# Optimization experiments

Measured on AMD Instinct MI355X. Metric: run time of the kernel, lower is better.

The kernel has to match this reference:

```python
import jax, jax.numpy as jnp
import numpy as np

DIM = 1024
STATE = 16
K = 4
INNER = 2048
BATCH = 4
SEQ = 2048
EPS = 1e-6


def silu(x):
    return x * jax.nn.sigmoid(x)


def setup_inputs() -> dict:
    key = jax.random.key(0)
    ks = jax.random.split(key, 8)
    g = lambda k, s, sc: jax.random.normal(k, s, dtype=jnp.float32) * sc
    return {
        "x": jax.random.normal(ks[0], (BATCH, SEQ, DIM), dtype=jnp.float32),
        "w_norm": jnp.ones((DIM,), jnp.float32),
        "W_in": g(ks[1], (2 * INNER, DIM), 0.02),
        "conv_w": g(ks[2], (INNER, K), 0.2),  # depthwise conv kernel
        "conv_b": jnp.zeros((INNER,), jnp.float32),
        "W_dt": g(ks[3], (INNER, INNER), 0.02),
        "b_dt": jnp.zeros((INNER,), jnp.float32),
        "W_B": g(ks[4], (STATE, INNER), 0.02),
        "W_C": g(ks[5], (STATE, INNER), 0.02),
        "A_log": jnp.log(jnp.broadcast_to(jnp.arange(1, STATE + 1, dtype=jnp.float32), (INNER, STATE))),
        "D": jnp.ones((INNER,), jnp.float32),
        "W_out": g(ks[6], (DIM, INNER), 0.02),
    }


def reference(x, w_norm, W_in, conv_w, conv_b, W_dt, b_dt, W_B, W_C, A_log, D, W_out):
    b, L, d = x.shape
    # RMSNorm
    x_norm = x * jax.lax.rsqrt(jnp.mean(x * x, axis=-1, keepdims=True) + EPS) * w_norm
    # input projection and split
    x_and_res = x_norm @ W_in.T  # (b, L, 2*inner)
    x_inner, res = jnp.split(x_and_res, 2, axis=-1)
    # causal depthwise conv1d (pad left K-1, kernel per channel)
    xp = jnp.pad(x_inner, ((0, 0), (K - 1, 0), (0, 0)))
    x_conv = sum(xp[:, j:j + L, :] * conv_w[:, j] for j in range(K)) + conv_b
    x_conv = silu(x_conv)
    # SSM parameters
    dt = jax.nn.softplus(x_conv @ W_dt.T + b_dt)  # (b, L, inner)
    Bm = x_conv @ W_B.T  # (b, L, state)
    Cm = x_conv @ W_C.T  # (b, L, state)
    A = -jnp.exp(A_log)  # (inner, state)

    def step(h, inp):
        dt_t, B_t, C_t, xc_t = inp  # (b,inner),(b,state),(b,state),(b,inner)
        dA = jnp.exp(A * dt_t[..., None])  # (b, inner, state)
        h = dA * h + (dt_t[..., None] * B_t[:, None, :]) * xc_t[..., None]
        y_t = jnp.einsum('bis,bs->bi', h, C_t) + D * xc_t
        return h, y_t

    h0 = jnp.zeros((b, INNER, STATE), x.dtype)
    xs = (dt.transpose(1, 0, 2), Bm.transpose(1, 0, 2), Cm.transpose(1, 0, 2), x_conv.transpose(1, 0, 2))
    _, y = jax.lax.scan(step, h0, xs)  # y: (L, b, inner)
    y = y.transpose(1, 0, 2)
    y = y * silu(res)
    return y @ W_out.T
```

## Files before the change

### kernel.cpp

```cpp
#include <hip/hip_runtime.h>


typedef __bf16 bf16;
typedef __attribute__((ext_vector_type(8))) __bf16 bf16x8;
typedef __attribute__((ext_vector_type(4))) float f32x4;

#define DIM   1024
#define STATE 16
#define INNER 2048
#define BATCH 4
#define SEQ   2048
#define ROWS  (BATCH * SEQ)
#define N1    (2 * INNER)
#define NBC   2176
#define CHUNK 128
#define NC    (SEQ / CHUNK)
#define PF2   4

#define GLOAD_LDS16(g, l)                                                  \
  __builtin_amdgcn_global_load_lds(                                        \
      (const __attribute__((address_space(1))) unsigned int*)(g),          \
      (__attribute__((address_space(3))) unsigned int*)(l), 16, 0, 0)

__global__ void ws_report_kernel(float* out, float wssz, float need) {
  if (threadIdx.x == 0) { out[0] = wssz; out[1] = need; }
}

__global__ __launch_bounds__(256) void rmsnorm_kernel(
    const float* __restrict__ x, const float* __restrict__ w,
    bf16* __restrict__ out) {
  const int row = blockIdx.x;
  const int t = threadIdx.x;
  const float4 v = ((const float4*)(x + (long)row * DIM))[t];
  float ss = v.x * v.x + v.y * v.y + v.z * v.z + v.w * v.w;
#pragma unroll
  for (int off = 32; off > 0; off >>= 1) ss += __shfl_xor(ss, off, 64);
  __shared__ float red[4];
  if ((t & 63) == 0) red[t >> 6] = ss;
  __syncthreads();
  const float tot = red[0] + red[1] + red[2] + red[3];
  const float scale = rsqrtf(tot * (1.0f / DIM) + 1e-6f);
  const float4 wv = ((const float4*)w)[t];
  bf16* o = out + (long)row * DIM + t * 4;
  o[0] = (bf16)(v.x * scale * wv.x);
  o[1] = (bf16)(v.y * scale * wv.y);
  o[2] = (bf16)(v.z * scale * wv.z);
  o[3] = (bf16)(v.w * scale * wv.w);
}

__global__ __launch_bounds__(256) void cvt_bf16_kernel(
    const float* __restrict__ src, bf16* __restrict__ dst, int n) {
  const int i = blockIdx.x * 256 + threadIdx.x;
  if (i < n) dst[i] = (bf16)src[i];
}

__global__ __launch_bounds__(256) void build_wdtbc_kernel(
    const float* __restrict__ Wdt, const float* __restrict__ WB,
    const float* __restrict__ WC, bf16* __restrict__ dst) {
  const long i = (long)blockIdx.x * 256 + threadIdx.x;
  const long r = i >> 11;
  const long k = i & (INNER - 1);
  float v = 0.0f;
  if (r < 2048) v = Wdt[r * INNER + k];
  else if (r < 2064) v = WB[(r - 2048) * INNER + k];
  else if (r < 2080) v = WC[(r - 2064) * INNER + k];
  dst[i] = (bf16)v;
}

__global__ __launch_bounds__(256) void build_a2_kernel(
    const float* __restrict__ A_log, float* __restrict__ A2) {
  const int i = blockIdx.x * 256 + threadIdx.x;
  A2[i] = -__expf(A_log[i]) * 1.4426950408889634f;
}

template <int EPI>
__global__ __launch_bounds__(256) void gemm_bf16_kernel(
    const bf16* __restrict__ A, const bf16* __restrict__ B,
    float* __restrict__ Cf, float* __restrict__ Cf2,
    bf16* __restrict__ Cb, bf16* __restrict__ Cb2,
    const float* __restrict__ bias, int nx, int N, int K) {
  __shared__ __align__(16) bf16 As[128 * 32];
  __shared__ __align__(16) bf16 Bs[128 * 32];
  const int tid = threadIdx.x;
  const int lane = tid & 63;
  const int wave = tid >> 6;

  const int per = gridDim.x >> 3;
  const int lin = (blockIdx.x & 7) * per + (blockIdx.x >> 3);
  const int row_t = lin / nx;
  const int col_t = lin - row_t * nx;
  const long row0 = (long)row_t * 128;
  const long col0 = (long)col_t * 128;

  const int wr = (wave >> 1) * 64;
  const int wc = (wave & 1) * 64;

  f32x4 acc[4][4];
#pragma unroll
  for (int i = 0; i < 4; i++)
#pragma unroll
    for (int j = 0; j < 4; j++) acc[i][j] = (f32x4){0.f, 0.f, 0.f, 0.f};

  const int srow = tid >> 2;
  const int scol = (tid & 3) * 8;
  const bf16* gA0 = A + (row0 + srow) * (long)K + scol;
  const bf16* gA1 = A + (row0 + srow + 64) * (long)K + scol;
  const bf16* gB0 = B + (col0 + srow) * (long)K + scol;
  const bf16* gB1 = B + (col0 + srow + 64) * (long)K + scol;
  bf16* lA0 = As + wave * 512 + lane * 8;
  bf16* lA1 = As + 64 * 32 + wave * 512 + lane * 8;
  bf16* lB0 = Bs + wave * 512 + lane * 8;
  bf16* lB1 = Bs + 64 * 32 + wave * 512 + lane * 8;

  const int fm = lane & 15;
  const int fk = (lane >> 4) * 8;

  for (int k0 = 0; k0 < K; k0 += 32) {
    GLOAD_LDS16(gA0 + k0, lA0);
    GLOAD_LDS16(gA1 + k0, lA1);
    GLOAD_LDS16(gB0 + k0, lB0);
    GLOAD_LDS16(gB1 + k0, lB1);
    __syncthreads();
    bf16x8 af[4], bfv[4];
#pragma unroll
    for (int i = 0; i < 4; i++)
      af[i] = *(const bf16x8*)(As + (wr + i * 16 + fm) * 32 + fk);
#pragma unroll
    for (int j = 0; j < 4; j++)
      bfv[j] = *(const bf16x8*)(Bs + (wc + j * 16 + fm) * 32 + fk);
#pragma unroll
    for (int i = 0; i < 4; i++)
#pragma unroll
      for (int j = 0; j < 4; j++)
        acc[i][j] = __builtin_amdgcn_mfma_f32_16x16x32_bf16(
            af[i], bfv[j], acc[i][j], 0, 0, 0);
    __syncthreads();
  }

  const int er = (lane >> 4) * 4;
  const int ec = lane & 15;
#pragma unroll
  for (int i = 0; i < 4; i++) {
#pragma unroll
    for (int j = 0; j < 4; j++) {
      const long col = col0 + wc + j * 16 + ec;
      const long rw = row0 + wr + i * 16 + er;
#pragma unroll
      for (int r = 0; r < 4; r++) {
        const float v = acc[i][j][r];
        const long row = rw + r;
        if (EPI == 0) {
          Cf[row * (long)N + col] = v;
        } else if (EPI == 1) {
          if (col0 < 2048) {
            float z = v + bias[col];
            z = (z > 20.0f) ? z : log1pf(__expf(z));
            Cf[row * 2048 + col] = z;
          } else if (col < 2080) {
            Cf2[row * 32 + (col - 2048)] = v;
          }
        } else {
          if (col0 < 2048) {
            Cb[row * 2048 + col] = (bf16)v;
          } else {
            const float s = v / (1.0f + __expf(-v));
            Cb2[row * 2048 + (col - 2048)] = (bf16)s;
          }
        }
      }
    }
  }
}

__global__ __launch_bounds__(256) void conv_silu_kernel(
    const bf16* __restrict__ xin, const float* __restrict__ conv_w,
    const float* __restrict__ conv_b, bf16* __restrict__ xc16) {
  const int c = blockIdx.x * 256 + threadIdx.x;
  const int r = blockIdx.y;
  const int l = r & (SEQ - 1);
  const float4 w = *(const float4*)(conv_w + c * 4);
  float acc = conv_b[c];
#pragma unroll
  for (int j = 0; j < 4; j++) {
    const int lp = l - 3 + j;
    const float xv = (lp >= 0) ? (float)xin[(long)(r - 3 + j) * INNER + c] : 0.0f;
    acc += xv * ((const float*)&w)[j];
  }
  const float s = acc / (1.0f + __expf(-acc));
  xc16[(long)r * INNER + c] = (bf16)s;
}

__global__ __launch_bounds__(256) void scan_pass1_kernel(
    const float* __restrict__ dtm, const float* __restrict__ bc,
    const bf16* __restrict__ xc, const float* __restrict__ A2,
    float* __restrict__ hend, float* __restrict__ dtsum) {
  const int ch = blockIdx.x * 256 + threadIdx.x;
  const int c = blockIdx.y;
  const int b = blockIdx.z;
  const long row0 = (long)b * SEQ + (long)c * CHUNK;

  float a2[16];
#pragma unroll
  for (int q = 0; q < 4; q++) {
    const float4 t = ((const float4*)(A2 + (long)ch * 16))[q];
    a2[q * 4 + 0] = t.x; a2[q * 4 + 1] = t.y;
    a2[q * 4 + 2] = t.z; a2[q * 4 + 3] = t.w;
  }
  float h[16];
#pragma unroll
  for (int s = 0; s < 16; s++) h[s] = 0.0f;
  float dts = 0.0f;

  float dtq[PF2], xcq[PF2];
#pragma unroll
  for (int p = 0; p < PF2; p++) {
    const long r2 = row0 + p;
    dtq[p] = dtm[r2 * INNER + ch];
    xcq[p] = (float)xc[r2 * INNER + ch];
  }
  for (int l0 = 0; l0 <= CHUNK - 2 * PF2; l0 += PF2) {
#pragma unroll
    for (int p = 0; p < PF2; p++) {
      const float dt = dtq[p], xcv = xcq[p];
      const long rp = row0 + l0 + p + PF2;
      dtq[p] = dtm[rp * INNER + ch];
      xcq[p] = (float)xc[rp * INNER + ch];
      const long r = row0 + l0 + p;
      float Bv[16];
#pragma unroll
      for (int k = 0; k < 16; k++) Bv[k] = bc[r * 32 + k];
      dts += dt;
      const float u = dt * xcv;
#pragma unroll
      for (int s = 0; s < 16; s++)
        h[s] = exp2f(a2[s] * dt) * h[s] + Bv[s] * u;
    }
  }
#pragma unroll
  for (int p = 0; p < PF2; p++) {
    const float dt = dtq[p], xcv = xcq[p];
    const long r = row0 + CHUNK - PF2 + p;
    float Bv[16];
#pragma unroll
    for (int k = 0; k < 16; k++) Bv[k] = bc[r * 32 + k];
    dts += dt;
    const float u = dt * xcv;
#pragma unroll
    for (int s = 0; s < 16; s++)
      h[s] = exp2f(a2[s] * dt) * h[s] + Bv[s] * u;
  }

  const long cb = (long)(b * NC + c);
#pragma unroll
  for (int s = 0; s < 16; s++) hend[(cb * 16 + s) * INNER + ch] = h[s];
  dtsum[cb * INNER + ch] = dts;
}

__global__ __launch_bounds__(256) void scan_combine_kernel(
    float* __restrict__ hio, const float* __restrict__ dtsum,
    const float* __restrict__ A2) {
  const int idx = blockIdx.x * 256 + threadIdx.x;
  const int ch = idx & (INNER - 1);
  const int s = (idx >> 11) & 15;
  const int b = idx >> 15;
  const float a2 = A2[(long)ch * 16 + s];
  float H = 0.0f;
  for (int c = 0; c < NC; c++) {
    const long cb = (long)(b * NC + c);
    const long o = (cb * 16 + s) * INNER + ch;
    const float he = hio[o];
    const float ds = dtsum[cb * INNER + ch];
    hio[o] = H;
    H = exp2f(a2 * ds) * H + he;
  }
}

__global__ __launch_bounds__(256) void scan_pass3_kernel(
    const float* __restrict__ dtm, const float* __restrict__ bc,
    const bf16* __restrict__ xc, const bf16* __restrict__ rs,
    const float* __restrict__ A2, const float* __restrict__ Dv,
    const float* __restrict__ hstart, bf16* __restrict__ y) {
  const int ch = blockIdx.x * 256 + threadIdx.x;
  const int c = blockIdx.y;
  const int b = blockIdx.z;
  const long row0 = (long)b * SEQ + (long)c * CHUNK;

  float a2[16];
#pragma unroll
  for (int q = 0; q < 4; q++) {
    const float4 t = ((const float4*)(A2 + (long)ch * 16))[q];
    a2[q * 4 + 0] = t.x; a2[q * 4 + 1] = t.y;
    a2[q * 4 + 2] = t.z; a2[q * 4 + 3] = t.w;
  }
  const float d = Dv[ch];
  const long cb = (long)(b * NC + c);
  float h[16];
#pragma unroll
  for (int s = 0; s < 16; s++) h[s] = hstart[(cb * 16 + s) * INNER + ch];

  float dtq[PF2], xcq[PF2], rsq[PF2];
#pragma unroll
  for (int p = 0; p < PF2; p++) {
    const long r2 = row0 + p;
    dtq[p] = dtm[r2 * INNER + ch];
    xcq[p] = (float)xc[r2 * INNER + ch];
    rsq[p] = (float)rs[r2 * INNER + ch];
  }
  for (int l0 = 0; l0 <= CHUNK - 2 * PF2; l0 += PF2) {
#pragma unroll
    for (int p = 0; p < PF2; p++) {
      const float dt = dtq[p], xcv = xcq[p], rsv = rsq[p];
      const long rp = row0 + l0 + p + PF2;
      dtq[p] = dtm[rp * INNER + ch];
      xcq[p] = (float)xc[rp * INNER + ch];
      rsq[p] = (float)rs[rp * INNER + ch];
      const long r = row0 + l0 + p;
      float Bv[16], Cv[16];
#pragma unroll
      for (int k = 0; k < 16; k++) Bv[k] = bc[r * 32 + k];
#pragma unroll
      for (int k = 0; k < 16; k++) Cv[k] = bc[r * 32 + 16 + k];
      const float u = dt * xcv;
      float yv = d * xcv;
#pragma unroll
      for (int s = 0; s < 16; s++) {
        h[s] = exp2f(a2[s] * dt) * h[s] + Bv[s] * u;
        yv += h[s] * Cv[s];
      }
      y[r * INNER + ch] = (bf16)(yv * rsv);
    }
  }
#pragma unroll
  for (int p = 0; p < PF2; p++) {
    const float dt = dtq[p], xcv = xcq[p], rsv = rsq[p];
    const long r = row0 + CHUNK - PF2 + p;
    float Bv[16], Cv[16];
#pragma unroll
    for (int k = 0; k < 16; k++) Bv[k] = bc[r * 32 + k];
#pragma unroll
    for (int k = 0; k < 16; k++) Cv[k] = bc[r * 32 + 16 + k];
    const float u = dt * xcv;
    float yv = d * xcv;
#pragma unroll
    for (int s = 0; s < 16; s++) {
      h[s] = exp2f(a2[s] * dt) * h[s] + Bv[s] * u;
      yv += h[s] * Cv[s];
    }
    y[r * INNER + ch] = (bf16)(yv * rsv);
  }
}

extern "C" void kernel_launch(void* const* d_in, const int* in_sizes, int n_in,
                              void* d_out, int out_size, void* d_ws,
                              size_t ws_size, hipStream_t stream) {
  (void)in_sizes; (void)n_in; (void)out_size;
  const float* x      = (const float*)d_in[0];
  const float* w_norm = (const float*)d_in[1];
  const float* W_in   = (const float*)d_in[2];
  const float* conv_w = (const float*)d_in[3];
  const float* conv_b = (const float*)d_in[4];
  const float* W_dt   = (const float*)d_in[5];
  const float* b_dt   = (const float*)d_in[6];
  const float* W_B    = (const float*)d_in[7];
  const float* W_C    = (const float*)d_in[8];
  const float* A_log  = (const float*)d_in[9];
  const float* Dv     = (const float*)d_in[10];
  const float* W_out  = (const float*)d_in[11];
  float* out = (float*)d_out;

  const size_t MB = 1024ull * 1024ull;
  char* base = (char*)d_ws;
  bf16*  xnorm  = (bf16*)(base + 0);
  bf16*  win_b  = (bf16*)(base + 16 * MB);
  bf16*  xin_b  = (bf16*)(base + 24 * MB);
  float* dtm    = (float*)(base + 0);
  float* bcm    = (float*)(base + 64 * MB);
  bf16*  res_b  = (bf16*)(base + 65 * MB);
  bf16*  xc_b   = (bf16*)(base + 97 * MB);
  bf16*  wdtbcb = (bf16*)(base + 129 * MB);
  float* hend   = (float*)(base + 129 * MB);
  float* dtsum  = (float*)(base + 137 * MB);
  char*  p2     = base + 129 * MB + (size_t)NBC * INNER * 2;
  bf16*  wout_b = (bf16*)p2;
  float* A2     = (float*)(p2 + (size_t)DIM * INNER * 2);
  bf16*  yb     = (bf16*)(p2 + (size_t)DIM * INNER * 2 +
                          (size_t)INNER * STATE * 4);
  const size_t NEEDED = (size_t)((char*)yb - base) + (size_t)ROWS * INNER * 2;

  if (ws_size < NEEDED) {
    ws_report_kernel<<<1, 64, 0, stream>>>(out, (float)ws_size, (float)NEEDED);
    return;
  }

  rmsnorm_kernel<<<ROWS, 256, 0, stream>>>(x, w_norm, xnorm);

  cvt_bf16_kernel<<<(N1 * DIM) / 256, 256, 0, stream>>>(W_in, win_b, N1 * DIM);
  build_wdtbc_kernel<<<(NBC * INNER) / 256, 256, 0, stream>>>(W_dt, W_B, W_C,
                                                              wdtbcb);
  cvt_bf16_kernel<<<(DIM * INNER) / 256, 256, 0, stream>>>(W_out, wout_b,
                                                           DIM * INNER);
  build_a2_kernel<<<(INNER * STATE) / 256, 256, 0, stream>>>(A_log, A2);

  gemm_bf16_kernel<2><<<(N1 / 128) * (ROWS / 128), 256, 0, stream>>>(
      xnorm, win_b, nullptr, nullptr, xin_b, res_b, nullptr, N1 / 128, N1,
      DIM);

  conv_silu_kernel<<<dim3(INNER / 256, ROWS), 256, 0, stream>>>(
      xin_b, conv_w, conv_b, xc_b);

  gemm_bf16_kernel<1><<<(NBC / 128) * (ROWS / 128), 256, 0, stream>>>(
      xc_b, wdtbcb, dtm, bcm, nullptr, nullptr, b_dt, NBC / 128, NBC, INNER);

  scan_pass1_kernel<<<dim3(INNER / 256, NC, BATCH), 256, 0, stream>>>(
      dtm, bcm, xc_b, A2, hend, dtsum);
  scan_combine_kernel<<<(BATCH * 16 * INNER) / 256, 256, 0, stream>>>(
      hend, dtsum, A2);
  scan_pass3_kernel<<<dim3(INNER / 256, NC, BATCH), 256, 0, stream>>>(
      dtm, bcm, xc_b, res_b, A2, Dv, hend, yb);

  gemm_bf16_kernel<0><<<(DIM / 128) * (ROWS / 128), 256, 0, stream>>>(
      yb, wout_b, out, nullptr, nullptr, nullptr, nullptr, DIM / 128, DIM,
      INNER);
}
```

Measured before the change: 713.6 us.

## Use 256x256 tiled bf16 GEMM with LDS double buffering for in-proj and dt/B/C GEMMs

Adds a new GEMM kernel with 256x256 output tiles, 512 threads (8 waves), and double-buffered LDS filled by direct global-to-LDS loads. The MFMA work is split into phases with staggered prefetch, barriers and s_setprio. It replaces the 128x128 GEMM for the input projection and the dt/B/C projection, keeping the fused epilogues (SiLU on res, softplus+bias, B/C output). The aim is more operand reuse per tile and loads overlapped with compute. The costs are 128KB of LDS per block, which limits occupancy, and the row clamp needed to handle B's padded 2176-row matrix.

```diff
diff --git a/kernel.cpp b/kernel.cpp
--- a/kernel.cpp
+++ b/kernel.cpp
@@ -71,6 +71,198 @@
     const float* __restrict__ A_log, float* __restrict__ A2) {
   const int i = blockIdx.x * 256 + threadIdx.x;
   A2[i] = -__expf(A_log[i]) * 1.4426950408889634f;
+}
+
+#define MFMA_PHASE(I0, N0)                                                    \
+  __builtin_amdgcn_s_barrier();                                               \
+  asm volatile("s_waitcnt lgkmcnt(0)" ::: "memory");                          \
+  __builtin_amdgcn_s_setprio(1);                                              \
+  _Pragma("unroll") for (int i_ = 0; i_ < 4; ++i_)                            \
+  _Pragma("unroll") for (int n_ = 0; n_ < 2; ++n_)                            \
+  _Pragma("unroll") for (int k_ = 0; k_ < 2; ++k_)                            \
+      acc[(I0) + i_][(N0) + n_] = __builtin_amdgcn_mfma_f32_16x16x32_bf16(    \
+          afr[i_][k_], bfr[(N0) + n_][k_], acc[(I0) + i_][(N0) + n_], 0, 0,   \
+          0);                                                                 \
+  __builtin_amdgcn_s_setprio(0);                                              \
+  __builtin_amdgcn_s_barrier();
+
+template <int EPI, int K, int NX>
+__global__ __launch_bounds__(512, 2) void gemm256_kernel(
+    const bf16* __restrict__ A, const bf16* __restrict__ B,
+    float* __restrict__ Cf, float* __restrict__ Cf2,
+    bf16* __restrict__ Cb, bf16* __restrict__ Cb2,
+    const float* __restrict__ bias, int Bmax) {
+  __shared__ __align__(16) char lds[2][65536];
+  const int tid = threadIdx.x;
+  const int lane = tid & 63;
+  const int wave = tid >> 6;
+  const int wm = wave >> 2;
+  const int wn = wave & 3;
+
+  const int per = gridDim.x >> 3;
+  const int lin = (blockIdx.x & 7) * per + (blockIdx.x >> 3);
+  const int row_t = lin / NX;
+  const int col_t = lin - row_t * NX;
+  const long row0 = (long)row_t * 256;
+  const long col0 = (long)col_t * 256;
+
+  const int srow = tid >> 3;
+  const int scb = (tid & 7) * 16;
+  const int sswz = scb ^ ((srow & 7) << 4);
+  const char* gA = (const char*)A + (row0 + srow) * (long)(2 * K) + sswz;
+  const char* gB = (const char*)B + sswz;
+  long brow[4];
+#pragma unroll
+  for (int q = 0; q < 4; ++q) {
+    long r = col0 + q * 64 + srow;
+    brow[q] = (r > (long)Bmax ? (long)Bmax : r) * (long)(2 * K);
+  }
+
+#define STG_A(bb, q, kbyte)                                                   \
+  GLOAD_LDS16(gA + (long)(q) * 64 * (2 * K) + (kbyte),                        \
+              lds[bb] + (q) * 8192 + srow * 128 + scb)
+#define STG_B(bb, q, kbyte)                                                   \
+  GLOAD_LDS16(gB + brow[q] + (kbyte),                                         \
+              lds[bb] + 32768 + (q) * 8192 + srow * 128 + scb)
+
+  const int fm = lane & 15;
+  const int fq = lane >> 4;
+  const int swz = (fm & 7) << 4;
+  const int ck0 = (fq * 16) ^ swz;
+  const int ck1 = (fq * 16 + 64) ^ swz;
+  const int aro = (wm * 128 + fm) * 128;
+  const int bro = (wn * 64 + fm) * 128;
+
+  f32x4 acc[8][4];
+#pragma unroll
+  for (int i = 0; i < 8; ++i)
+#pragma unroll
+    for (int n = 0; n < 4; ++n) acc[i][n] = (f32x4){0.f, 0.f, 0.f, 0.f};
+  bf16x8 afr[4][2], bfr[4][2];
+
+  const int NT = K / 64;
+#pragma unroll
+  for (int q = 0; q < 4; ++q) STG_A(0, q, 0);
+#pragma unroll
+  for (int q = 0; q < 4; ++q) STG_B(0, q, 0);
+
+  for (int t = 0; t < NT; ++t) {
+    const int c = t & 1;
+    const int nb = c ^ 1;
+    const char* Ac = lds[c];
+    const char* Bc = lds[c] + 32768;
+    const long kb = (long)(t + 1) * 128;
+    const bool nx = (t + 1 < NT);
+    if (nx) {
+      STG_A(nb, 0, kb);
+      STG_A(nb, 1, kb);
+      asm volatile("s_waitcnt vmcnt(2)" ::: "memory");
+    } else {
+      asm volatile("s_waitcnt vmcnt(0)" ::: "memory");
+    }
+    __builtin_amdgcn_s_barrier();
+    asm volatile("" ::: "memory");
+#pragma unroll
+    for (int i = 0; i < 4; ++i) {
+      afr[i][0] = *(const bf16x8*)(Ac + aro + i * 2048 + ck0);
+      afr[i][1] = *(const bf16x8*)(Ac + aro + i * 2048 + ck1);
+    }
+#pragma unroll
+    for (int n = 0; n < 2; ++n) {
+      bfr[n][0] = *(const bf16x8*)(Bc + bro + n * 2048 + ck0);
+      bfr[n][1] = *(const bf16x8*)(Bc + bro + n * 2048 + ck1);
+    }
+    if (nx) { STG_A(nb, 2, kb); STG_A(nb, 3, kb); }
+    MFMA_PHASE(0, 0)
+#pragma unroll
+    for (int n = 2; n < 4; ++n) {
+      bfr[n][0] = *(const bf16x8*)(Bc + bro + n * 2048 + ck0);
+      bfr[n][1] = *(const bf16x8*)(Bc + bro + n * 2048 + ck1);
+    }
+    if (nx) { STG_B(nb, 0, kb); STG_B(nb, 1, kb); }
+    MFMA_PHASE(0, 2)
+#pragma unroll
+    for (int i = 0; i < 4; ++i) {
+      afr[i][0] = *(const bf16x8*)(Ac + aro + 8192 + i * 2048 + ck0);
+      afr[i][1] = *(const bf16x8*)(Ac + aro + 8192 + i * 2048 + ck1);
+    }
+    if (nx) { STG_B(nb, 2, kb); STG_B(nb, 3, kb); }
+    MFMA_PHASE(4, 2)
+    __builtin_amdgcn_s_setprio(1);
+#pragma unroll
+    for (int i = 0; i < 4; ++i)
+#pragma unroll
+      for (int n = 0; n < 2; ++n)
+#pragma unroll
+        for (int kk = 0; kk < 2; ++kk)
+          acc[4 + i][n] = __builtin_amdgcn_mfma_f32_16x16x32_bf16(
+              afr[i][kk], bfr[n][kk], acc[4 + i][n], 0, 0, 0);
+    __builtin_amdgcn_s_setprio(0);
+    __builtin_amdgcn_s_barrier();
+    asm volatile("" ::: "memory");
+  }
+#undef STG_A
+#undef STG_B
+
+  const int er = fq * 4;
+  const long rbase = row0 + wm * 128;
+  const long cbase = col0 + wn * 64;
+  if (EPI == 2) {
+    if (col0 < 2048) {
+#pragma unroll
+      for (int i = 0; i < 8; ++i)
+#pragma unroll
+        for (int n = 0; n < 4; ++n) {
+          const long col = cbase + n * 16 + fm;
+          const long rw = rbase + i * 16 + er;
+#pragma unroll
+          for (int r = 0; r < 4; ++r)
+            Cb[(rw + r) * 2048 + col] = (bf16)acc[i][n][r];
+        }
+    } else {
+#pragma unroll
+      for (int i = 0; i < 8; ++i)
+#pragma unroll
+        for (int n = 0; n < 4; ++n) {
+          const long col = cbase + n * 16 + fm - 2048;
+          const long rw = rbase + i * 16 + er;
+#pragma unroll
+          for (int r = 0; r < 4; ++r) {
+            const float v = acc[i][n][r];
+            const float s = v / (1.0f + __expf(-v));
+            Cb2[(rw + r) * 2048 + col] = (bf16)s;
+          }
+        }
+    }
+  } else {
+    if (col0 < 2048) {
+#pragma unroll
+      for (int i = 0; i < 8; ++i)
+#pragma unroll
+        for (int n = 0; n < 4; ++n) {
+          const long col = cbase + n * 16 + fm;
+          const float bs = bias[col];
+          const long rw = rbase + i * 16 + er;
+#pragma unroll
+          for (int r = 0; r < 4; ++r) {
+            float z = acc[i][n][r] + bs;
+            z = (z > 20.0f) ? z : log1pf(__expf(z));
+            Cf[(rw + r) * 2048 + col] = z;
+          }
+        }
+    } else if (wn == 0) {
+#pragma unroll
+      for (int i = 0; i < 8; ++i)
+#pragma unroll
+        for (int n = 0; n < 2; ++n) {
+          const long col = n * 16 + fm;
+          const long rw = rbase + i * 16 + er;
+#pragma unroll
+          for (int r = 0; r < 4; ++r)
+            Cf2[(rw + r) * 32 + col] = acc[i][n][r];
+        }
+    }
+  }
 }
 
 template <int EPI>
@@ -401,15 +593,14 @@
                                                            DIM * INNER);
   build_a2_kernel<<<(INNER * STATE) / 256, 256, 0, stream>>>(A_log, A2);
 
-  gemm_bf16_kernel<2><<<(N1 / 128) * (ROWS / 128), 256, 0, stream>>>(
-      xnorm, win_b, nullptr, nullptr, xin_b, res_b, nullptr, N1 / 128, N1,
-      DIM);
+  gemm256_kernel<2, 1024, 16><<<512, 512, 0, stream>>>(
+      xnorm, win_b, nullptr, nullptr, xin_b, res_b, nullptr, N1 - 1);
 
   conv_silu_kernel<<<dim3(INNER / 256, ROWS), 256, 0, stream>>>(
       xin_b, conv_w, conv_b, xc_b);
 
-  gemm_bf16_kernel<1><<<(NBC / 128) * (ROWS / 128), 256, 0, stream>>>(
-      xc_b, wdtbcb, dtm, bcm, nullptr, nullptr, b_dt, NBC / 128, NBC, INNER);
+  gemm256_kernel<1, 2048, 9><<<288, 512, 0, stream>>>(
+      xc_b, wdtbcb, dtm, bcm, nullptr, nullptr, b_dt, NBC - 1);
 
   scan_pass1_kernel<<<dim3(INNER / 256, NC, BATCH), 256, 0, stream>>>(
       dtm, bcm, xc_b, A2, hend, dtsum);
```

Measured after the change: 648.9 us. 1.1x faster.

## Add 256x256 multi-buffered GEMM kernel and split dt/BC projection

Applied to the files above, without the earlier changes.

Introduces a 512-thread GEMM with 256x256 tiles, a 4-stage LDS ring filled by direct global-to-LDS loads, XOR swizzling, and priority hints around MFMA bursts. It is used for the input projection, the dt projection and the output projection. The dt GEMM is split from the B/C projection, so the padded 2176-wide tile no longer wastes work. The small B/C GEMM now runs as a separate narrow launch. The goal is more operand reuse per tile and better latency hiding than the 128x128 single-buffered kernel, at the cost of more registers and fewer blocks (128 for the output GEMM).

```diff
diff --git a/kernel.cpp b/kernel.cpp
--- a/kernel.cpp
+++ b/kernel.cpp
@@ -54,16 +54,15 @@
   if (i < n) dst[i] = (bf16)src[i];
 }
 
-__global__ __launch_bounds__(256) void build_wdtbc_kernel(
-    const float* __restrict__ Wdt, const float* __restrict__ WB,
-    const float* __restrict__ WC, bf16* __restrict__ dst) {
-  const long i = (long)blockIdx.x * 256 + threadIdx.x;
-  const long r = i >> 11;
-  const long k = i & (INNER - 1);
+__global__ __launch_bounds__(256) void build_wbc_kernel(
+    const float* __restrict__ WB, const float* __restrict__ WC,
+    bf16* __restrict__ dst) {
+  const int i = blockIdx.x * 256 + threadIdx.x;
+  const int r = i >> 11;
+  const int k = i & (INNER - 1);
   float v = 0.0f;
-  if (r < 2048) v = Wdt[r * INNER + k];
-  else if (r < 2064) v = WB[(r - 2048) * INNER + k];
-  else if (r < 2080) v = WC[(r - 2064) * INNER + k];
+  if (r < 16) v = WB[r * INNER + k];
+  else if (r < 32) v = WC[(r - 16) * INNER + k];
   dst[i] = (bf16)v;
 }
 
@@ -73,12 +72,173 @@
   A2[i] = -__expf(A_log[i]) * 1.4426950408889634f;
 }
 
+template <int EPI, int K, int NX>
+__global__ __launch_bounds__(512, 2) void gemm256_kernel(
+    const bf16* __restrict__ A, const bf16* __restrict__ B,
+    float* __restrict__ Cf, bf16* __restrict__ Cb, bf16* __restrict__ Cb2,
+    const float* __restrict__ bias) {
+  __shared__ __align__(16) char lds[4][32768];
+  const int tid = threadIdx.x;
+  const int lane = tid & 63;
+  const int wave = tid >> 6;
+  const int wm = wave >> 2;
+  const int wn = wave & 3;
+
+  const int per = gridDim.x >> 3;
+  const int lin = (blockIdx.x & 7) * per + (blockIdx.x >> 3);
+  const int row_t = lin / NX;
+  const int col_t = lin - row_t * NX;
+  const long row0 = (long)row_t * 256;
+  const long col0 = (long)col_t * 256;
+
+  const int srow = tid >> 2;
+  const int scb = (tid & 3) * 16;
+  const int ssw = scb ^ (((srow >> 1) & 3) << 4);
+  const char* gA = (const char*)A + (row0 + srow) * (long)(2 * K) + ssw;
+  const char* gB = (const char*)B + (col0 + srow) * (long)(2 * K) + ssw;
+
+#define STG_A(bb, r, tt)                                                      \
+  GLOAD_LDS16(gA + (long)(r) * 128 * (2 * K) + (long)(tt) * 64,               \
+              lds[bb] + (r) * 8192 + srow * 64 + scb)
+#define STG_B(bb, r, tt)                                                      \
+  GLOAD_LDS16(gB + (long)(r) * 128 * (2 * K) + (long)(tt) * 64,               \
+              lds[bb] + 16384 + (r) * 8192 + srow * 64 + scb)
+
+  const int fm = lane & 15;
+  const int fq = lane >> 4;
+  const int ck = (fq * 16) ^ (((fm >> 1) & 3) << 4);
+  const int aro = (wm * 128 + fm) * 64;
+  const int bro = (wn * 64 + fm) * 64;
+
+  f32x4 acc[8][4];
+#pragma unroll
+  for (int i = 0; i < 8; ++i)
+#pragma unroll
+    for (int n = 0; n < 4; ++n) acc[i][n] = (f32x4){0.f, 0.f, 0.f, 0.f};
+  bf16x8 afr[4], bfr[4];
+
+  const int NT = K / 32;
+#pragma unroll
+  for (int t = 0; t < 3; ++t) {
+    STG_A(t, 0, t); STG_A(t, 1, t);
+    STG_B(t, 0, t); STG_B(t, 1, t);
+  }
+  asm volatile("s_waitcnt vmcnt(8)" ::: "memory");
+  __builtin_amdgcn_s_barrier();
+
+  for (int t = 0; t < NT; ++t) {
+    const int c = t & 3;
+    const int pb = (t + 3) & 3;
+    const char* Ac = lds[c];
+    const char* Bc = lds[c] + 16384;
+    const bool pf = (t + 3) < NT;
+#pragma unroll
+    for (int i = 0; i < 4; ++i)
+      afr[i] = *(const bf16x8*)(Ac + aro + i * 1024 + ck);
+#pragma unroll
+    for (int n = 0; n < 4; ++n)
+      bfr[n] = *(const bf16x8*)(Bc + bro + n * 1024 + ck);
+    if (pf) { STG_A(pb, 0, t + 3); STG_A(pb, 1, t + 3); }
+    __builtin_amdgcn_s_barrier();
+    asm volatile("s_waitcnt lgkmcnt(0)" ::: "memory");
+    __builtin_amdgcn_s_setprio(1);
+#pragma unroll
+    for (int i = 0; i < 4; ++i)
+#pragma unroll
+      for (int n = 0; n < 4; ++n)
+        acc[i][n] = __builtin_amdgcn_mfma_f32_16x16x32_bf16(
+            afr[i], bfr[n], acc[i][n], 0, 0, 0);
+    __builtin_amdgcn_s_setprio(0);
+    __builtin_amdgcn_s_barrier();
+#pragma unroll
+    for (int i = 0; i < 4; ++i)
+      afr[i] = *(const bf16x8*)(Ac + aro + (i + 4) * 1024 + ck);
+    if (pf) { STG_B(pb, 0, t + 3); STG_B(pb, 1, t + 3); }
+    __builtin_amdgcn_s_barrier();
+    asm volatile("s_waitcnt lgkmcnt(0)" ::: "memory");
+    __builtin_amdgcn_s_setprio(1);
+#pragma unroll
+    for (int i = 0; i < 4; ++i)
+#pragma unroll
+      for (int n = 0; n < 4; ++n)
+        acc[4 + i][n] = __builtin_amdgcn_mfma_f32_16x16x32_bf16(
+            afr[i], bfr[n], acc[4 + i][n], 0, 0, 0);
+    __builtin_amdgcn_s_setprio(0);
+    if (t < NT - 3) {
+      asm volatile("s_waitcnt vmcnt(8)" ::: "memory");
+    } else if (t == NT - 3) {
+      asm volatile("s_waitcnt vmcnt(4)" ::: "memory");
+    } else if (t == NT - 2) {
+      asm volatile("s_waitcnt vmcnt(0)" ::: "memory");
+    }
+    __builtin_amdgcn_s_barrier();
+  }
+#undef STG_A
+#undef STG_B
+
+  const int er = fq * 4;
+  const long rbase = row0 + wm * 128;
+  const long cbase = col0 + wn * 64;
+  if (EPI == 0) {
+    const long Nn = 256 * NX;
+#pragma unroll
+    for (int i = 0; i < 8; ++i)
+#pragma unroll
+      for (int n = 0; n < 4; ++n) {
+        const long col = cbase + n * 16 + fm;
+        const long rw = rbase + i * 16 + er;
+#pragma unroll
+        for (int r = 0; r < 4; ++r) Cf[(rw + r) * Nn + col] = acc[i][n][r];
+      }
+  } else if (EPI == 1) {
+#pragma unroll
+    for (int i = 0; i < 8; ++i)
+#pragma unroll
+      for (int n = 0; n < 4; ++n) {
+        const long col = cbase + n * 16 + fm;
+        const float bs = bias[col];
+        const long rw = rbase + i * 16 + er;
+#pragma unroll
+        for (int r = 0; r < 4; ++r) {
+          float z = acc[i][n][r] + bs;
+          z = (z > 20.0f) ? z : log1pf(__expf(z));
+          Cf[(rw + r) * 2048 + col] = z;
+        }
+      }
+  } else {
+    if (col0 < 2048) {
+#pragma unroll
+      for (int i = 0; i < 8; ++i)
+#pragma unroll
+        for (int n = 0; n < 4; ++n) {
+          const long col = cbase + n * 16 + fm;
+          const long rw = rbase + i * 16 + er;
+#pragma unroll
+          for (int r = 0; r < 4; ++r)
+            Cb[(rw + r) * 2048 + col] = (bf16)acc[i][n][r];
+        }
+    } else {
+#pragma unroll
+      for (int i = 0; i < 8; ++i)
+#pragma unroll
+        for (int n = 0; n < 4; ++n) {
+          const long col = cbase + n * 16 + fm - 2048;
+          const long rw = rbase + i * 16 + er;
+#pragma unroll
+          for (int r = 0; r < 4; ++r) {
+            const float v = acc[i][n][r];
+            const float s = v / (1.0f + __expf(-v));
+            Cb2[(rw + r) * 2048 + col] = (bf16)s;
+          }
+        }
+    }
+  }
+}
+
 template <int EPI>
 __global__ __launch_bounds__(256) void gemm_bf16_kernel(
     const bf16* __restrict__ A, const bf16* __restrict__ B,
-    float* __restrict__ Cf, float* __restrict__ Cf2,
-    bf16* __restrict__ Cb, bf16* __restrict__ Cb2,
-    const float* __restrict__ bias, int nx, int N, int K) {
+    float* __restrict__ Cf2, int nx, int N, int K) {
   __shared__ __align__(16) bf16 As[128 * 32];
   __shared__ __align__(16) bf16 Bs[128 * 32];
   const int tid = threadIdx.x;
@@ -149,23 +309,8 @@
       for (int r = 0; r < 4; r++) {
         const float v = acc[i][j][r];
         const long row = rw + r;
-        if (EPI == 0) {
-          Cf[row * (long)N + col] = v;
-        } else if (EPI == 1) {
-          if (col0 < 2048) {
-            float z = v + bias[col];
-            z = (z > 20.0f) ? z : log1pf(__expf(z));
-            Cf[row * 2048 + col] = z;
-          } else if (col < 2080) {
-            Cf2[row * 32 + (col - 2048)] = v;
-          }
-        } else {
-          if (col0 < 2048) {
-            Cb[row * 2048 + col] = (bf16)v;
-          } else {
-            const float s = v / (1.0f + __expf(-v));
-            Cb2[row * 2048 + (col - 2048)] = (bf16)s;
-          }
+        if (EPI == 3) {
+          if (col < 32) Cf2[row * 32 + col] = v;
         }
       }
     }
@@ -377,7 +522,8 @@
   float* bcm    = (float*)(base + 64 * MB);
   bf16*  res_b  = (bf16*)(base + 65 * MB);
   bf16*  xc_b   = (bf16*)(base + 97 * MB);
-  bf16*  wdtbcb = (bf16*)(base + 129 * MB);
+  bf16*  wdt_b  = (bf16*)(base + 129 * MB);
+  bf16*  wbc_b  = (bf16*)(base + 137 * MB);
   float* hend   = (float*)(base + 129 * MB);
   float* dtsum  = (float*)(base + 137 * MB);
   char*  p2     = base + 129 * MB + (size_t)NBC * INNER * 2;
@@ -395,21 +541,23 @@
   rmsnorm_kernel<<<ROWS, 256, 0, stream>>>(x, w_norm, xnorm);
 
   cvt_bf16_kernel<<<(N1 * DIM) / 256, 256, 0, stream>>>(W_in, win_b, N1 * DIM);
-  build_wdtbc_kernel<<<(NBC * INNER) / 256, 256, 0, stream>>>(W_dt, W_B, W_C,
-                                                              wdtbcb);
+  cvt_bf16_kernel<<<(INNER * INNER) / 256, 256, 0, stream>>>(W_dt, wdt_b,
+                                                             INNER * INNER);
+  build_wbc_kernel<<<(128 * INNER) / 256, 256, 0, stream>>>(W_B, W_C, wbc_b);
   cvt_bf16_kernel<<<(DIM * INNER) / 256, 256, 0, stream>>>(W_out, wout_b,
                                                            DIM * INNER);
   build_a2_kernel<<<(INNER * STATE) / 256, 256, 0, stream>>>(A_log, A2);
 
-  gemm_bf16_kernel<2><<<(N1 / 128) * (ROWS / 128), 256, 0, stream>>>(
-      xnorm, win_b, nullptr, nullptr, xin_b, res_b, nullptr, N1 / 128, N1,
-      DIM);
+  gemm256_kernel<2, 1024, 16><<<512, 512, 0, stream>>>(
+      xnorm, win_b, nullptr, xin_b, res_b, nullptr);
 
   conv_silu_kernel<<<dim3(INNER / 256, ROWS), 256, 0, stream>>>(
       xin_b, conv_w, conv_b, xc_b);
 
-  gemm_bf16_kernel<1><<<(NBC / 128) * (ROWS / 128), 256, 0, stream>>>(
-      xc_b, wdtbcb, dtm, bcm, nullptr, nullptr, b_dt, NBC / 128, NBC, INNER);
+  gemm256_kernel<1, 2048, 8><<<256, 512, 0, stream>>>(
+      xc_b, wdt_b, dtm, nullptr, nullptr, b_dt);
+
+  gemm_bf16_kernel<3><<<64, 256, 0, stream>>>(xc_b, wbc_b, bcm, 1, 128, INNER);
 
   scan_pass1_kernel<<<dim3(INNER / 256, NC, BATCH), 256, 0, stream>>>(
       dtm, bcm, xc_b, A2, hend, dtsum);
@@ -418,7 +566,6 @@
   scan_pass3_kernel<<<dim3(INNER / 256, NC, BATCH), 256, 0, stream>>>(
       dtm, bcm, xc_b, res_b, A2, Dv, hend, yb);
 
-  gemm_bf16_kernel<0><<<(DIM / 128) * (ROWS / 128), 256, 0, stream>>>(
-      yb, wout_b, out, nullptr, nullptr, nullptr, nullptr, DIM / 128, DIM,
-      INNER);
-}
+  gemm256_kernel<0, 2048, 4><<<128, 512, 0, stream>>>(
+      yb, wout_b, out, nullptr, nullptr, nullptr);
+}
```

Measured after the change: 668.1 us. -6.4%, faster.
